# Kernel optimization log

Measured on AMD Instinct MI355X. Metric: run time of the kernel, lower is better.

Reference implementation:

```python
import jax, jax.numpy as jnp
import numpy as np

FILL = -1024.0


def setup_inputs() -> dict:
    key = jax.random.key(0)
    ks = jax.random.split(key, 8)
    B, Q, K, D, KD, VD = 4, 4096, 4096, 512, 64, 64
    s = 0.02  # small init scale for numeric sanity
    return {
        "x": jax.random.normal(ks[0], (B, Q, D), dtype=jnp.float32),
        "buffer": jax.random.normal(ks[1], (B, K, D), dtype=jnp.float32),
        "mask": jax.random.randint(ks[2], (B, Q, K), 0, 2) > 0,
        "Wq": jax.random.normal(ks[3], (KD, D), dtype=jnp.float32) * s,
        "bq": jnp.zeros((KD,), dtype=jnp.float32),
        "Wk": jax.random.normal(ks[4], (KD, D), dtype=jnp.float32) * s,
        "bk": jnp.zeros((KD,), dtype=jnp.float32),
        "Wv": jax.random.normal(ks[5], (VD, D), dtype=jnp.float32) * s,
        "bv": jnp.zeros((VD,), dtype=jnp.float32),
    }


def reference(x, buffer, mask, Wq, bq, Wk, bk, Wv, bv):
    key_dim = Wq.shape[0]
    query = x @ Wq.T + bq          # [B, Q, KD]
    keys = buffer @ Wk.T + bk      # [B, K, KD]
    vals = buffer @ Wv.T + bv      # [B, K, VD]
    logits = jnp.einsum('bqd,bkd->bqk', query, keys) / np.sqrt(key_dim).astype(np.float32)
    logits = jnp.where(mask, logits, FILL)
    # stable softmax (same math as exp(x - max) / sum)
    probs = jax.nn.softmax(logits, axis=-1)
    read = jnp.einsum('bqk,bkd->bqd', probs, vals)  # [B, Q, VD]
    return read
```

## Files before the change

### kernel.cpp

```cpp
#include <hip/hip_runtime.h>
#include <hip/hip_bf16.h>

typedef float f32x4 __attribute__((ext_vector_type(4)));
typedef __bf16 bf16x8 __attribute__((ext_vector_type(8)));

#define NB 4
#define NQ 4096
#define NK 4096
#define DIM 512
#define KD 64
#define PKW 128

#define PACK_BLOCKS 8192

__device__ inline bf16x8 load_cvt8(const float* __restrict__ p) {
    float4 f0 = *(const float4*)p;
    float4 f1 = *(const float4*)(p + 4);
    bf16x8 r;
    r[0] = (__bf16)f0.x; r[1] = (__bf16)f0.y; r[2] = (__bf16)f0.z; r[3] = (__bf16)f0.w;
    r[4] = (__bf16)f1.x; r[5] = (__bf16)f1.y; r[6] = (__bf16)f1.z; r[7] = (__bf16)f1.w;
    return r;
}

__global__ __launch_bounds__(256, 4) void prep_kernel(
        const float* __restrict__ x, const float* __restrict__ buf,
        const int* __restrict__ mask,
        const float* __restrict__ Wq, const float* __restrict__ bq,
        const float* __restrict__ Wk, const float* __restrict__ bk,
        const float* __restrict__ Wv, const float* __restrict__ bv,
        __bf16* __restrict__ Qb, __bf16* __restrict__ Kb, __bf16* __restrict__ Vt,
        unsigned* __restrict__ pk) {
    __shared__ __align__(16) float ps[4][32][66];

    const int tid = threadIdx.x;

    if (blockIdx.x < PACK_BLOCKS) {
        long t = (long)blockIdx.x * 256 + tid;
        const int4* p4 = (const int4*)(mask + t * 32);
        unsigned r = 0;
#pragma unroll
        for (int j = 0; j < 8; j++) {
            int4 v = p4[j];
            r |= (v.x ? 1u : 0u) << (j * 4 + 0);
            r |= (v.y ? 1u : 0u) << (j * 4 + 1);
            r |= (v.z ? 1u : 0u) << (j * 4 + 2);
            r |= (v.w ? 1u : 0u) << (j * 4 + 3);
        }
        pk[t] = r;
        return;
    }

    const int w = tid >> 6, l = tid & 63;
    const int lr = l & 15, lk = l >> 4;
    const int rg = w >> 1, kh = w & 1;
    const bool is_q = blockIdx.x < PACK_BLOCKS + 512;
    const int blk = is_q ? blockIdx.x - PACK_BLOCKS : blockIdx.x - PACK_BLOCKS - 512;
    const long rowbase = (long)blk * 32 + rg * 16;
    const int kbase = kh * 256;

    if (is_q) {
        f32x4 acc[4] = {};
        for (int kk = 0; kk < 256; kk += 32) {
            bf16x8 a = load_cvt8(x + (rowbase + lr) * DIM + kbase + kk + lk * 8);
#pragma unroll
            for (int nb = 0; nb < 4; nb++) {
                bf16x8 bw = load_cvt8(Wq + (long)(nb * 16 + lr) * DIM + kbase + kk + lk * 8);
                acc[nb] = __builtin_amdgcn_mfma_f32_16x16x32_bf16(a, bw, acc[nb], 0, 0, 0);
            }
        }
#pragma unroll
        for (int nb = 0; nb < 4; nb++)
#pragma unroll
            for (int i = 0; i < 4; i++)
                ps[kh * 2][rg * 16 + lk * 4 + i][nb * 16 + lr] = acc[nb][i];
        __syncthreads();
        for (int e = tid; e < 2048; e += 256) {
            int row = e >> 6, col = e & 63;
            float v = ps[0][row][col] + ps[2][row][col] + bq[col];
            Qb[((long)blk * 32 + row) * KD + col] = (__bf16)v;
        }
    } else {
        f32x4 acck[4] = {}, accv[4] = {};
        for (int kk = 0; kk < 256; kk += 32) {
            bf16x8 a = load_cvt8(buf + (rowbase + lr) * DIM + kbase + kk + lk * 8);
#pragma unroll
            for (int nb = 0; nb < 4; nb++) {
                bf16x8 bwk = load_cvt8(Wk + (long)(nb * 16 + lr) * DIM + kbase + kk + lk * 8);
                bf16x8 bwv = load_cvt8(Wv + (long)(nb * 16 + lr) * DIM + kbase + kk + lk * 8);
                acck[nb] = __builtin_amdgcn_mfma_f32_16x16x32_bf16(a, bwk, acck[nb], 0, 0, 0);
                accv[nb] = __builtin_amdgcn_mfma_f32_16x16x32_bf16(a, bwv, accv[nb], 0, 0, 0);
            }
        }
#pragma unroll
        for (int nb = 0; nb < 4; nb++)
#pragma unroll
            for (int i = 0; i < 4; i++) {
                ps[kh * 2 + 0][rg * 16 + lk * 4 + i][nb * 16 + lr] = acck[nb][i];
                ps[kh * 2 + 1][rg * 16 + lk * 4 + i][nb * 16 + lr] = accv[nb][i];
            }
        __syncthreads();
        for (int e = tid; e < 2048; e += 256) {
            int row = e >> 6, col = e & 63;
            float v = ps[0][row][col] + ps[2][row][col] + bk[col];
            Kb[((long)blk * 32 + row) * KD + col] = (__bf16)v;
        }
        for (int e = tid; e < 2048; e += 256) {
            int row = e & 31, col = e >> 5;
            float v = ps[1][row][col] + ps[3][row][col] + bv[col];
            long grow = (long)blk * 32 + row;
            int b = (int)(grow >> 12), kidx = (int)(grow & 4095);
            Vt[((long)b * KD + col) * NK + kidx] = (__bf16)v;
        }
    }
}

__global__ __launch_bounds__(256, 4) void attn_kernel(
        const __bf16* __restrict__ Qb, const __bf16* __restrict__ Kb,
        const __bf16* __restrict__ Vt, const unsigned* __restrict__ pk,
        float* __restrict__ out) {
    __shared__ __align__(16) char smem[18432];

    const int tid = threadIdx.x;
    const int w = tid >> 6, l = tid & 63;
    const int lr = l & 15, lk = l >> 4;
    const int b = blockIdx.x >> 8;
    const int q0 = (blockIdx.x & 255) * 16;
    const int k0 = w * 1024;

    const __bf16* Qp = Qb + ((long)b * NQ + q0) * KD;
    const __bf16* Kp = Kb + (long)b * NK * KD;
    const __bf16* Vp = Vt + (long)b * KD * NK;
    const unsigned* mp = pk + ((long)b * NQ + q0) * PKW;

    __bf16 (*pl0)[72] = (__bf16(*)[72])(smem + w * 4608);
    __bf16 (*pl1)[72] = (__bf16(*)[72])(smem + w * 4608 + 2304);

    bf16x8 qa[2];
#pragma unroll
    for (int ks = 0; ks < 2; ks++)
        qa[ks] = *(const bf16x8*)(Qp + (long)lr * KD + ks * 32 + lk * 8);

    f32x4 o[4] = {};
    float l_i[4] = {0.f, 0.f, 0.f, 0.f};

    auto tile = [&](int kt, __bf16 (*pl)[72]) {
        f32x4 s[4] = {};
#pragma unroll
        for (int ks = 0; ks < 2; ks++)
#pragma unroll
            for (int nb = 0; nb < 4; nb++) {
                bf16x8 kb = *(const bf16x8*)(Kp + (long)(kt + nb * 16 + lr) * KD + ks * 32 + lk * 8);
                s[nb] = __builtin_amdgcn_mfma_f32_16x16x32_bf16(qa[ks], kb, s[nb], 0, 0, 0);
            }
        unsigned mw0[4], mw1[4];
#pragma unroll
        for (int i = 0; i < 4; i++) {
            uint2 mwv = *(const uint2*)(mp + (long)(lk * 4 + i) * PKW + (kt >> 5));
            mw0[i] = mwv.x; mw1[i] = mwv.y;
        }
#pragma unroll
        for (int nb = 0; nb < 4; nb++) {
            const unsigned bit = (unsigned)((nb * 16 + lr) & 31);
#pragma unroll
            for (int i = 0; i < 4; i++) {
                unsigned wv = (nb < 2) ? mw0[i] : mw1[i];
                float e = __expf(s[nb][i] * 0.125f);
                float p = ((wv >> bit) & 1u) ? e : 0.0f;
                __bf16 pb = (__bf16)p;
                pl[lk * 4 + i][nb * 16 + lr] = pb;
                l_i[i] += (float)pb;
            }
        }
#pragma unroll
        for (int ks = 0; ks < 2; ks++) {
            bf16x8 pa = *(const bf16x8*)&pl[lr][ks * 32 + lk * 8];
#pragma unroll
            for (int nb = 0; nb < 4; nb++) {
                bf16x8 vb = *(const bf16x8*)(Vp + (long)(nb * 16 + lr) * NK + kt + ks * 32 + lk * 8);
                o[nb] = __builtin_amdgcn_mfma_f32_16x16x32_bf16(pa, vb, o[nb], 0, 0, 0);
            }
        }
    };

#pragma unroll 1
    for (int kt = k0; kt < k0 + 1024; kt += 128) {
        tile(kt, pl0);
        tile(kt + 64, pl1);
    }

#pragma unroll
    for (int i = 0; i < 4; i++) {
        float v = l_i[i];
        v += __shfl_xor(v, 1);
        v += __shfl_xor(v, 2);
        v += __shfl_xor(v, 4);
        v += __shfl_xor(v, 8);
        l_i[i] = v;
    }

    __syncthreads();
    float* o_s = (float*)smem;
    float* ml  = (float*)(smem + 4 * 16 * 66 * 4);
#pragma unroll
    for (int nb = 0; nb < 4; nb++)
#pragma unroll
        for (int i = 0; i < 4; i++)
            o_s[(w * 16 + lk * 4 + i) * 66 + nb * 16 + lr] = o[nb][i];
    if (lr == 0) {
#pragma unroll
        for (int i = 0; i < 4; i++)
            ml[w * 16 + lk * 4 + i] = l_i[i];
    }
    __syncthreads();
    for (int e = tid; e < 1024; e += 256) {
        int row = e >> 6, col = e & 63;
        float L = ml[row] + ml[16 + row] + ml[32 + row] + ml[48 + row];
        float O = 0.f;
#pragma unroll
        for (int ww = 0; ww < 4; ww++)
            O += o_s[(ww * 16 + row) * 66 + col];
        out[((long)b * NQ + q0 + row) * KD + col] = O / L;
    }
}

extern "C" void kernel_launch(void* const* d_in, const int* in_sizes, int n_in,
                              void* d_out, int out_size, void* d_ws, size_t ws_size,
                              hipStream_t stream) {
    const float* x      = (const float*)d_in[0];
    const float* buffer = (const float*)d_in[1];
    const int*   mask   = (const int*)d_in[2];
    const float* Wq     = (const float*)d_in[3];
    const float* bq     = (const float*)d_in[4];
    const float* Wk     = (const float*)d_in[5];
    const float* bk     = (const float*)d_in[6];
    const float* Wv     = (const float*)d_in[7];
    const float* bv     = (const float*)d_in[8];
    float* out = (float*)d_out;

    unsigned* pk = (unsigned*)d_ws;
    __bf16* Qb = (__bf16*)((char*)d_ws + (size_t)NB * NQ * PKW * 4);
    __bf16* Kb = Qb + (size_t)NB * NQ * KD;
    __bf16* Vt = Kb + (size_t)NB * NK * KD;

    prep_kernel<<<dim3(PACK_BLOCKS + 1024), dim3(256), 0, stream>>>(
        x, buffer, mask, Wq, bq, Wk, bk, Wv, bv, Qb, Kb, Vt, pk);
    attn_kernel<<<dim3(NB * (NQ / 16)), dim3(256), 0, stream>>>(Qb, Kb, Vt, pk, out);
}
```

Measured before the change: 236.1 us.

## Pack mask with wave ballots and split attention keys across 8 waves

The mask packing now uses wave-wide ballot instructions: each wave reads coalesced int rows and writes 64-bit bitmasks, replacing per-thread 32-int strided gathers. Fewer packing blocks loop over the mask, and the projection blocks move to the front of the grid. The attention kernel doubles its block to 512 threads, so each of 8 waves handles 512 keys instead of 1024. This adds parallelism and latency hiding per query tile, at the cost of double the shared memory and a larger cross-wave reduction.

Result: faster. 226.1 us (-4.2%).

```diff
diff --git a/kernel.cpp b/kernel.cpp
--- a/kernel.cpp
+++ b/kernel.cpp
@@ -3,6 +3,8 @@
 
 typedef float f32x4 __attribute__((ext_vector_type(4)));
 typedef __bf16 bf16x8 __attribute__((ext_vector_type(8)));
+typedef unsigned long long u64;
+typedef u64 u64x2 __attribute__((ext_vector_type(2)));
 
 #define NB 4
 #define NQ 4096
@@ -10,8 +12,9 @@
 #define DIM 512
 #define KD 64
 #define PKW 128
-
-#define PACK_BLOCKS 8192
+#define NG64 (1 << 20)
+#define PACK_BLOCKS 2048
+#define PACK_WAVES (PACK_BLOCKS * 4)
 
 __device__ inline bf16x8 load_cvt8(const float* __restrict__ p) {
     float4 f0 = *(const float4*)p;
@@ -33,28 +36,34 @@
     __shared__ __align__(16) float ps[4][32][66];
 
     const int tid = threadIdx.x;
-
-    if (blockIdx.x < PACK_BLOCKS) {
-        long t = (long)blockIdx.x * 256 + tid;
-        const int4* p4 = (const int4*)(mask + t * 32);
-        unsigned r = 0;
-#pragma unroll
-        for (int j = 0; j < 8; j++) {
-            int4 v = p4[j];
-            r |= (v.x ? 1u : 0u) << (j * 4 + 0);
-            r |= (v.y ? 1u : 0u) << (j * 4 + 1);
-            r |= (v.z ? 1u : 0u) << (j * 4 + 2);
-            r |= (v.w ? 1u : 0u) << (j * 4 + 3);
-        }
-        pk[t] = r;
+    const int w = tid >> 6, l = tid & 63;
+
+    if (blockIdx.x >= 1024) {
+        const int wid = (blockIdx.x - 1024) * 4 + w;
+        u64* pk64 = (u64*)pk;
+        for (int g0 = wid * 4; g0 < NG64; g0 += PACK_WAVES * 4) {
+            const int* mb = mask + (long)g0 * 64 + l;
+            int m0 = mb[0];
+            int m1 = mb[64];
+            int m2 = mb[128];
+            int m3 = mb[192];
+            u64 b0 = __ballot(m0 != 0);
+            u64 b1 = __ballot(m1 != 0);
+            u64 b2 = __ballot(m2 != 0);
+            u64 b3 = __ballot(m3 != 0);
+            if (l == 0) {
+                u64x2 v01 = {b0, b1}, v23 = {b2, b3};
+                *(u64x2*)(pk64 + g0)     = v01;
+                *(u64x2*)(pk64 + g0 + 2) = v23;
+            }
+        }
         return;
     }
 
-    const int w = tid >> 6, l = tid & 63;
     const int lr = l & 15, lk = l >> 4;
     const int rg = w >> 1, kh = w & 1;
-    const bool is_q = blockIdx.x < PACK_BLOCKS + 512;
-    const int blk = is_q ? blockIdx.x - PACK_BLOCKS : blockIdx.x - PACK_BLOCKS - 512;
+    const bool is_q = blockIdx.x < 512;
+    const int blk = is_q ? blockIdx.x : blockIdx.x - 512;
     const long rowbase = (long)blk * 32 + rg * 16;
     const int kbase = kh * 256;
 
@@ -114,18 +123,18 @@
     }
 }
 
-__global__ __launch_bounds__(256, 4) void attn_kernel(
+__global__ __launch_bounds__(512, 4) void attn_kernel(
         const __bf16* __restrict__ Qb, const __bf16* __restrict__ Kb,
         const __bf16* __restrict__ Vt, const unsigned* __restrict__ pk,
         float* __restrict__ out) {
-    __shared__ __align__(16) char smem[18432];
+    __shared__ __align__(16) char smem[36864];
 
     const int tid = threadIdx.x;
     const int w = tid >> 6, l = tid & 63;
     const int lr = l & 15, lk = l >> 4;
     const int b = blockIdx.x >> 8;
     const int q0 = (blockIdx.x & 255) * 16;
-    const int k0 = w * 1024;
+    const int k0 = w * 512;
 
     const __bf16* Qp = Qb + ((long)b * NQ + q0) * KD;
     const __bf16* Kp = Kb + (long)b * NK * KD;
@@ -183,7 +192,7 @@
     };
 
 #pragma unroll 1
-    for (int kt = k0; kt < k0 + 1024; kt += 128) {
+    for (int kt = k0; kt < k0 + 512; kt += 128) {
         tile(kt, pl0);
         tile(kt + 64, pl1);
     }
@@ -200,7 +209,7 @@
 
     __syncthreads();
     float* o_s = (float*)smem;
-    float* ml  = (float*)(smem + 4 * 16 * 66 * 4);
+    float* ml  = (float*)(smem + 8 * 16 * 66 * 4);
 #pragma unroll
     for (int nb = 0; nb < 4; nb++)
 #pragma unroll
@@ -212,13 +221,14 @@
             ml[w * 16 + lk * 4 + i] = l_i[i];
     }
     __syncthreads();
-    for (int e = tid; e < 1024; e += 256) {
+    for (int e = tid; e < 1024; e += 512) {
         int row = e >> 6, col = e & 63;
-        float L = ml[row] + ml[16 + row] + ml[32 + row] + ml[48 + row];
-        float O = 0.f;
-#pragma unroll
-        for (int ww = 0; ww < 4; ww++)
+        float L = 0.f, O = 0.f;
+#pragma unroll
+        for (int ww = 0; ww < 8; ww++) {
+            L += ml[ww * 16 + row];
             O += o_s[(ww * 16 + row) * 66 + col];
+        }
         out[((long)b * NQ + q0 + row) * KD + col] = O / L;
     }
 }
@@ -242,7 +252,7 @@
     __bf16* Kb = Qb + (size_t)NB * NQ * KD;
     __bf16* Vt = Kb + (size_t)NB * NK * KD;
 
-    prep_kernel<<<dim3(PACK_BLOCKS + 1024), dim3(256), 0, stream>>>(
+    prep_kernel<<<dim3(1024 + PACK_BLOCKS), dim3(256), 0, stream>>>(
         x, buffer, mask, Wq, bq, Wk, bk, Wv, bv, Qb, Kb, Vt, pk);
-    attn_kernel<<<dim3(NB * (NQ / 16)), dim3(256), 0, stream>>>(Qb, Kb, Vt, pk, out);
-}
+    attn_kernel<<<dim3(NB * (NQ / 16)), dim3(512), 0, stream>>>(Qb, Kb, Vt, pk, out);
+}
```
